# Kernel optimization log

Measured on AMD Instinct MI355X. Metric: run time of the kernel, lower is better.

## Reference

```python
import jax, jax.numpy as jnp
import numpy as np

B, S_SRC, T, D, H, DFF, NC, L = 8, 256, 64, 256, 8, 1024, 128, 2
HD = D // H
EPS = 1e-5


def _pe(length, d):
    pos = jnp.arange(length, dtype=jnp.float32)[:, None]
    div = jnp.exp(jnp.arange(0, d, 2, dtype=jnp.float32) * (-np.log(10000.0) / d))
    pe = jnp.zeros((length, d), dtype=jnp.float32)
    pe = pe.at[:, 0::2].set(jnp.sin(pos * div))
    pe = pe.at[:, 1::2].set(jnp.cos(pos * div))
    return pe


def setup_inputs() -> dict:
    key = jax.random.key(0)
    ks = jax.random.split(key, 16)
    s = 0.02
    rn = lambda k, shape: jax.random.normal(k, shape, dtype=jnp.float32) * s
    return {
        "encoder_output": jax.random.normal(ks[0], (B, S_SRC, D), dtype=jnp.float32),
        "emb_w": rn(ks[1], (D, NC)), "emb_b": jnp.zeros((D,), jnp.float32),
        "sa_wqkv": rn(ks[2], (L, 3 * D, D)), "sa_bqkv": jnp.zeros((L, 3 * D), jnp.float32),
        "sa_wo": rn(ks[3], (L, D, D)), "sa_bo": jnp.zeros((L, D), jnp.float32),
        "ca_wqkv": rn(ks[4], (L, 3 * D, D)), "ca_bqkv": jnp.zeros((L, 3 * D), jnp.float32),
        "ca_wo": rn(ks[5], (L, D, D)), "ca_bo": jnp.zeros((L, D), jnp.float32),
        "ln1_g": jnp.ones((L, D), jnp.float32), "ln1_b": jnp.zeros((L, D), jnp.float32),
        "ln2_g": jnp.ones((L, D), jnp.float32), "ln2_b": jnp.zeros((L, D), jnp.float32),
        "ffn_w1": rn(ks[6], (L, DFF, D)), "ffn_b1": jnp.zeros((L, DFF), jnp.float32),
        "ffn_w2": rn(ks[7], (L, D, DFF)), "ffn_b2": jnp.zeros((L, D), jnp.float32),
        "ln3_g": jnp.ones((L, D), jnp.float32), "ln3_b": jnp.zeros((L, D), jnp.float32),
        "op_w1": rn(ks[8], (D, D)), "op_b1": jnp.zeros((D,), jnp.float32),
        "bn_g": jnp.ones((D,), jnp.float32), "bn_b": jnp.zeros((D,), jnp.float32),
        "op_w2": rn(ks[9], (NC, D)), "op_b2": jnp.zeros((NC,), jnp.float32),
        "tgt_length": T,
    }


def _ln(x, g, b):
    m = x.mean(-1, keepdims=True)
    v = ((x - m) ** 2).mean(-1, keepdims=True)
    return (x - m) * jax.lax.rsqrt(v + EPS) * g + b


def _heads(x):  # [B,T,D] -> [B,H,T,HD]
    b, t, _ = x.shape
    return x.reshape(b, t, H, HD).transpose(0, 2, 1, 3)


def _merge(x):  # [B,H,T,HD] -> [B,T,D]
    return x.transpose(0, 2, 1, 3).reshape(x.shape[0], -1, D)


def _forward(encoder_output, emb_w, emb_b, sa_wqkv, sa_bqkv, sa_wo, sa_bo,
             ca_wqkv, ca_bqkv, ca_wo, ca_bo, ln1_g, ln1_b, ln2_g, ln2_b,
             ffn_w1, ffn_b1, ffn_w2, ffn_b2, ln3_g, ln3_b,
             op_w1, op_b1, bn_g, bn_b, op_w2, op_b2, tgt_length):
    Tq = tgt_length
    pe = _pe(Tq, D)
    scale = 1.0 / np.sqrt(HD)
    causal = jnp.where(jnp.arange(Tq)[:, None] >= jnp.arange(Tq)[None, :], 0.0, -1e9).astype(jnp.float32)
    # cross-attention K/V from encoder memory (constant across decode steps)
    mem_kv = jnp.einsum('bsd,led->lbse', encoder_output, ca_wqkv[:, D:, :]) + ca_bqkv[:, None, None, D:]
    mem_k = mem_kv[..., :D].reshape(L, B, S_SRC, H, HD).transpose(0, 1, 3, 2, 4)
    mem_v = mem_kv[..., D:].reshape(L, B, S_SRC, H, HD).transpose(0, 1, 3, 2, 4)

    def decode_full(buf):  # buf [B,Tq,NC] -> logits [B,Tq,NC]
        x = buf @ emb_w.T + emb_b + pe[None]
        for l in range(L):
            qkv = x @ sa_wqkv[l].T + sa_bqkv[l]
            q, k, v = (_heads(qkv[..., i * D:(i + 1) * D]) for i in range(3))
            att = jax.nn.softmax(jnp.einsum('bhqe,bhke->bhqk', q, k) * scale + causal, axis=-1)
            o = _merge(jnp.einsum('bhqk,bhke->bhqe', att, v)) @ sa_wo[l].T + sa_bo[l]
            x = _ln(x + o, ln1_g[l], ln1_b[l])
            qc = _heads(x @ ca_wqkv[l, :D].T + ca_bqkv[l, :D])
            attc = jax.nn.softmax(jnp.einsum('bhqe,bhke->bhqk', qc, mem_k[l]) * scale, axis=-1)
            oc = _merge(jnp.einsum('bhqk,bhke->bhqe', attc, mem_v[l])) @ ca_wo[l].T + ca_bo[l]
            x = _ln(x + oc, ln2_g[l], ln2_b[l])
            f = jax.nn.relu(x @ ffn_w1[l].T + ffn_b1[l]) @ ffn_w2[l].T + ffn_b2[l]
            x = _ln(x + f, ln3_g[l], ln3_b[l])
        y = x @ op_w1.T + op_b1
        # eval-mode BatchNorm1d with running stats (0, 1): pure affine
        y = jax.nn.relu(y * (1.0 / np.sqrt(1.0 + EPS)) * bn_g + bn_b)
        return y @ op_w2.T + op_b2

    def step(buf, t):
        out = decode_full(buf)                                   # [B,Tq,NC]
        y_t = jax.lax.dynamic_slice_in_dim(out, t, 1, axis=1)    # [B,1,NC]
        buf = jax.lax.dynamic_update_slice_in_dim(buf, y_t, jnp.minimum(t + 1, Tq - 1), axis=1)
        return buf, y_t[:, 0]

    buf0 = jnp.zeros((B, Tq, NC), dtype=jnp.float32)  # decoder_input starts as zeros
    _, ys = jax.lax.scan(step, buf0, jnp.arange(Tq))
    return ys.transpose(1, 0, 2)  # [B,Tq,NC]


def reference(encoder_output, emb_w, emb_b, sa_wqkv, sa_bqkv, sa_wo, sa_bo,
              ca_wqkv, ca_bqkv, ca_wo, ca_bo, ln1_g, ln1_b, ln2_g, ln2_b,
              ffn_w1, ffn_b1, ffn_w2, ffn_b2, ln3_g, ln3_b,
              op_w1, op_b1, bn_g, bn_b, op_w2, op_b2, tgt_length):
    return _forward(encoder_output, emb_w, emb_b, sa_wqkv, sa_bqkv, sa_wo, sa_bo,
                    ca_wqkv, ca_bqkv, ca_wo, ca_bo, ln1_g, ln1_b, ln2_g, ln2_b,
                    ffn_w1, ffn_b1, ffn_w2, ffn_b2, ln3_g, ln3_b,
                    op_w1, op_b1, bn_g, bn_b, op_w2, op_b2, tgt_length)
```

## Files before the change

### kernel.cpp

```cpp
#include <hip/hip_runtime.h>
#include <math.h>


#define EPS_ 1e-5f
#define SCALE_ 0.17677669529663687f
#define BNS 0.99999500003749969f
#define DEV __device__ __forceinline__
#define DYNF 36864

#define D4(a,b) ((a).x*(b).x+(a).y*(b).y+(a).z*(b).z+(a).w*(b).w)
#define F4(p)  (*(float4*)(p))
#define CF4(p) (*(const float4*)(p))

DEV float ald(const float* p){return __hip_atomic_load(p,__ATOMIC_RELAXED,__HIP_MEMORY_SCOPE_AGENT);}
DEV void  ast(float* p,float v){__hip_atomic_store(p,v,__ATOMIC_RELAXED,__HIP_MEMORY_SCOPE_AGENT);}
DEV int   aldi(const int* p){return __hip_atomic_load(p,__ATOMIC_RELAXED,__HIP_MEMORY_SCOPE_AGENT);}
DEV void  asti(int* p,int v){__hip_atomic_store(p,v,__ATOMIC_RELAXED,__HIP_MEMORY_SCOPE_AGENT);}

DEV float wsum(float v){
#pragma unroll
  for(int o=32;o;o>>=1) v+=__shfl_xor(v,o,64);
  return v;
}
DEV float wmax(float v){
#pragma unroll
  for(int o=32;o;o>>=1) v=fmaxf(v,__shfl_xor(v,o,64));
  return v;
}

DEV void waitflags(const int* base,int n,int s){
  if((int)threadIdx.x<64){
    const int* p=base+threadIdx.x*32;
    bool need=(int)threadIdx.x<n;
    int v=need?aldi(p):0x7fffffff;
    while(!__all(v>=s)){ v=need?aldi(p):0x7fffffff; }
  }
  __syncthreads();
}

template<int NB>
DEV void ln_reg(float (&v)[NB],const float* __restrict__ g,
                const float* __restrict__ bb,float* red){
  int tid=threadIdx.x,wid=tid>>6,lane=tid&63;
  float s[NB],s2[NB];
#pragma unroll
  for(int r=0;r<NB;++r){ s[r]=wsum(v[r]); s2[r]=wsum(v[r]*v[r]); }
  if(lane==0){
#pragma unroll
    for(int r=0;r<NB;++r){ red[r*4+wid]=s[r]; red[NB*4+r*4+wid]=s2[r]; }
  }
  __syncthreads();
  float gv=g[tid],bv=bb[tid];
#pragma unroll
  for(int r=0;r<NB;++r){
    float S=red[r*4+0]+red[r*4+1]+red[r*4+2]+red[r*4+3];
    float S2=red[NB*4+r*4+0]+red[NB*4+r*4+1]+red[NB*4+r*4+2]+red[NB*4+r*4+3];
    float m=S*(1.f/256.f);
    float rs=rsqrtf(S2*(1.f/256.f)-m*m+EPS_);
    v[r]=(v[r]-m)*rs*gv+bv;
  }
}

template<int NB,int L>
DEV void role_s1(float* LDS,int h,int bs,
    const float* __restrict__ sa_wqkv,const float* __restrict__ sa_bqkv,
    const float* __restrict__ sa_wo,
    const float* __restrict__ ln2_g,const float* __restrict__ ln2_b,
    const float* __restrict__ ln3_g,const float* __restrict__ ln3_b,
    const float* __restrict__ ffn_b2,const float* __restrict__ emb_b,
    int* F1,const int* F3,const int* FX0,
    float* kc,float* vc,const float* r2red,float* r3red,
    const float* p3,float* p1,const float* xrow){
  const int tid=threadIdx.x;
  float* W   =LDS;
  float* WO  =LDS+24960;
  float* XS  =LDS+34176;
  float* QKV =LDS+35200;
  float* SC  =LDS+35584;
  float* PART=LDS+35840;
  float* RED =LDS+36096;

  for(int idx=tid;idx<96*64;idx+=256){
    int row=idx>>6,i4=idx&63,which=row>>5,j=row&31;
    F4(&W[row*260+4*i4])=CF4(sa_wqkv+(size_t)L*196608+((size_t)(which*256+h*32+j))*256+4*i4);
  }
  for(int idx=tid;idx<256*8;idx+=256){
    int c=idx>>3,i=idx&7;
    F4(&WO[c*36+4*i])=CF4(sa_wo+(size_t)L*65536+(size_t)c*256+h*32+4*i);
  }
  __syncthreads();

  float dv=expf((float)(tid&~1)*(-9.210340371976184f/256.f));

  for(int t=0;t<64;++t){
    if(L==0){
      waitflags(FX0+bs*32,NB,t);
      float aarg=(float)t*dv;
      float peb=emb_b[tid]+((tid&1)?cosf(aarg):sinf(aarg));
#pragma unroll
      for(int bi=0;bi<NB;++bi) XS[bi*256+tid]=ald(xrow+(bs+bi)*256+tid)+peb;
      __syncthreads();
    }else{
      waitflags(F3+bs*16*32,NB*16,t+1);
      float r2v[NB],p3v[NB][16];
#pragma unroll
      for(int bi=0;bi<NB;++bi) r2v[bi]=ald(r2red+(bs+bi)*256+tid);
#pragma unroll
      for(int bi=0;bi<NB;++bi)
#pragma unroll
        for(int cg=0;cg<16;++cg) p3v[bi][cg]=ald(p3+(cg*8+bs+bi)*256+tid);
      ln_reg<NB>(r2v,ln2_g,ln2_b,RED);
      float r3v[NB];
      float fb=ffn_b2[tid];
#pragma unroll
      for(int bi=0;bi<NB;++bi){
        float s=0.f;
#pragma unroll
        for(int cg=0;cg<16;++cg) s+=p3v[bi][cg];
        r3v[bi]=r2v[bi]+s+fb;
        if(h==0) ast(r3red+(bs+bi)*256+tid,r3v[bi]);
      }
      ln_reg<NB>(r3v,ln3_g,ln3_b,RED+32);
#pragma unroll
      for(int bi=0;bi<NB;++bi) XS[bi*256+tid]=r3v[bi];
      __syncthreads();
    }
    if(tid<192){
      int row=tid>>1,kq=tid&1;
      float a[NB];
#pragma unroll
      for(int bi=0;bi<NB;++bi) a[bi]=0.f;
#pragma unroll
      for(int i=0;i<32;++i){
        float4 w=F4(&W[row*260+kq*128+4*i]);
#pragma unroll
        for(int bi=0;bi<NB;++bi) a[bi]+=D4(w,F4(&XS[bi*256+kq*128+4*i]));
      }
#pragma unroll
      for(int bi=0;bi<NB;++bi) a[bi]+=__shfl_down(a[bi],1,64);
      if(kq==0){
        int which=row>>5,j=row&31;
        float bias=sa_bqkv[L*768+which*256+h*32+j];
#pragma unroll
        for(int bi=0;bi<NB;++bi){
          float v=a[bi]+bias;
          if(which==0) QKV[bi*96+j]=v;
          else{
            int off=(which==1)?32:64;
            QKV[bi*96+off+j]=v;
            float* cache=(which==1)?kc:vc;
            cache[(((size_t)L*64+(bs+bi)*8+h)*64+t)*32+j]=v;
          }
        }
      }
    }
    __syncthreads();
    {
      int bi=(tid>>6)&(NB-1),key=tid&63;
      float s=-3.0e38f;
      if(key<=t){
        float a=0.f;
        if(key==t){
#pragma unroll
          for(int i=0;i<8;++i) a+=D4(F4(&QKV[bi*96+4*i]),F4(&QKV[bi*96+32+4*i]));
        }else{
          const float4* kr=(const float4*)(kc+(((size_t)L*64+(bs+bi)*8+h)*64+key)*32);
#pragma unroll
          for(int i=0;i<8;++i) a+=D4(F4(&QKV[bi*96+4*i]),kr[i]);
        }
        s=a*SCALE_;
      }
      float mx=wmax(s);
      float e=(key<=t)?expf(s-mx):0.f;
      float sm=wsum(e);
      SC[bi*64+key]=e/sm;
    }
    __syncthreads();
    {
      int bi=(tid>>6)&(NB-1),lane=tid&63,gg=lane>>5,col=lane&31;
      float acc=0.f;
      int k0=gg*32,k1=min(k0+32,t+1);
      for(int k=k0;k<k1;++k){
        float vv=(k==t)?QKV[bi*96+64+col]
                       :vc[(((size_t)L*64+(bs+bi)*8+h)*64+k)*32+col];
        acc+=SC[bi*64+k]*vv;
      }
      PART[bi*64+gg*32+col]=acc;
    }
    __syncthreads();
    if(tid<NB*32){
      int bi=tid>>5,col=tid&31;
      QKV[bi*96+col]=PART[bi*64+col]+PART[bi*64+32+col];
    }
    __syncthreads();
    {
      float a[NB];
#pragma unroll
      for(int bi=0;bi<NB;++bi) a[bi]=0.f;
#pragma unroll
      for(int i=0;i<8;++i){
        float4 w=F4(&WO[tid*36+4*i]);
#pragma unroll
        for(int bi=0;bi<NB;++bi) a[bi]+=D4(w,F4(&QKV[bi*96+4*i]));
      }
#pragma unroll
      for(int bi=0;bi<NB;++bi) ast(p1+(h*8+bs+bi)*256+tid,a[bi]);
    }
    __syncthreads();
    if(tid<NB) asti(F1+((L*8+bs+tid)*8+h)*32,t+1);
  }
}

DEV void role_s2(float* LDS,int rid,
    const float* __restrict__ enc,
    const float* __restrict__ ca_wqkv,const float* __restrict__ ca_bqkv,
    const float* __restrict__ ca_wo,
    const float* __restrict__ ln1_g,const float* __restrict__ ln1_b,
    const float* __restrict__ ln3_g,const float* __restrict__ ln3_b,
    const float* __restrict__ sa_bo,const float* __restrict__ emb_b,
    const int* F1,int* F2,
    const float* r3red,float* r1red,const float* p1,float* p2,const float* xrow){
  const int tid=threadIdx.x;
  const int b=rid>>4,h=(rid>>1)&7,l=rid&1;
  float* WQ  =LDS;
  float* WO  =LDS+8320;
  float* MK  =LDS+17536;
  float* MV  =LDS+26752;
  float* XS  =LDS+35968;
  float* PS  =LDS+36224;
  float* PART=LDS+36480;
  float* QC  =LDS+36736;
  float* RED =LDS+36784;

  for(int idx=tid;idx<64*64;idx+=256){
    int row=idx>>6,i4=idx&63;
    int grow=(row<32)?(256+h*32+row):(512+h*32+row-32);
    F4(&LDS[row*260+4*i4])=CF4(ca_wqkv+(size_t)l*196608+(size_t)grow*256+4*i4);
  }
  __syncthreads();
  for(int p=0;p<2;++p){
    int s=p*128+(tid>>1),kh=tid&1;
    float4 er[32];
#pragma unroll
    for(int i=0;i<32;++i) er[i]=CF4(enc+((size_t)(b*256+s))*256+kh*128+4*i);
    for(int out=0;out<64;++out){
      float a=0.f;
#pragma unroll
      for(int i=0;i<32;++i) a+=D4(F4(&LDS[out*260+kh*128+4*i]),er[i]);
      a+=__shfl_down(a,1,64);
      if(kh==0){
        if(out<32) MK[s*36+out]    =a+ca_bqkv[l*768+256+h*32+out];
        else       MV[s*36+out-32] =a+ca_bqkv[l*768+512+h*32+out-32];
      }
    }
  }
  __syncthreads();
  for(int idx=tid;idx<32*64;idx+=256){
    int row=idx>>6,i4=idx&63;
    F4(&WQ[row*260+4*i4])=CF4(ca_wqkv+(size_t)l*196608+(size_t)(h*32+row)*256+4*i4);
  }
  for(int idx=tid;idx<256*8;idx+=256){
    int c=idx>>3,i=idx&7;
    F4(&WO[c*36+4*i])=CF4(ca_wo+(size_t)l*65536+(size_t)c*256+h*32+4*i);
  }
  __syncthreads();

  float dv=expf((float)(tid&~1)*(-9.210340371976184f/256.f));

  for(int t=0;t<64;++t){
    waitflags(F1+(l*8+b)*8*32,8,t+1);
    float p1v[8];
#pragma unroll
    for(int h2=0;h2<8;++h2) p1v[h2]=ald(p1+(h2*8+b)*256+tid);
    float xv;
    if(l==0){
      float aarg=(float)t*dv;
      xv=ald(xrow+b*256+tid)+emb_b[tid]+((tid&1)?cosf(aarg):sinf(aarg));
    }else{
      float t0[1]={ald(r3red+b*256+tid)};
      ln_reg<1>(t0,ln3_g,ln3_b,RED);
      xv=t0[0];
    }
    float r1v=xv+sa_bo[l*256+tid];
#pragma unroll
    for(int h2=0;h2<8;++h2) r1v+=p1v[h2];
    if(h==0) ast(r1red+l*2048+b*256+tid,r1v);
    float t1[1]={r1v};
    ln_reg<1>(t1,ln1_g+l*256,ln1_b+l*256,RED+32);
    XS[tid]=t1[0];
    __syncthreads();
    {
      int col=tid>>3,g=tid&7;
      float a=0.f;
#pragma unroll
      for(int i=0;i<8;++i) a+=D4(F4(&WQ[col*260+g*32+4*i]),F4(&XS[g*32+4*i]));
      a+=__shfl_down(a,4,64);a+=__shfl_down(a,2,64);a+=__shfl_down(a,1,64);
      if(g==0) QC[col]=a+ca_bqkv[l*768+h*32+col];
    }
    __syncthreads();
    {
      float a=0.f;
#pragma unroll
      for(int i=0;i<8;++i) a+=D4(F4(&MK[tid*36+4*i]),F4(&QC[4*i]));
      float sv=a*SCALE_;
      int wid=tid>>6,lane=tid&63;
      float mx=wmax(sv);
      if(lane==0) RED[wid]=mx;
      __syncthreads();
      mx=fmaxf(fmaxf(RED[0],RED[1]),fmaxf(RED[2],RED[3]));
      float e=expf(sv-mx);
      float sm=wsum(e);
      if(lane==0) RED[4+wid]=sm;
      __syncthreads();
      sm=RED[4]+RED[5]+RED[6]+RED[7];
      PS[tid]=e/sm;
    }
    __syncthreads();
    {
      int gg=tid>>5,col=tid&31;
      float acc=0.f;
      for(int s2=gg*32;s2<gg*32+32;++s2) acc+=PS[s2]*MV[s2*36+col];
      PART[gg*32+col]=acc;
    }
    __syncthreads();
    if(tid<32){
      float o=0.f;
#pragma unroll
      for(int g2=0;g2<8;++g2) o+=PART[g2*32+tid];
      QC[tid]=o;
    }
    __syncthreads();
    {
      float a=0.f;
#pragma unroll
      for(int i=0;i<8;++i) a+=D4(F4(&WO[tid*36+4*i]),F4(&QC[4*i]));
      ast(p2+(h*8+b)*256+tid,a);
    }
    __syncthreads();
    if(tid==0) asti(F2+((l*8+b)*8+h)*32,t+1);
  }
}

DEV void role_s3(float* LDS,int rid,
    const float* __restrict__ ffn_w1,const float* __restrict__ ffn_b1,
    const float* __restrict__ ffn_w2,
    const float* __restrict__ ln1_g,const float* __restrict__ ln1_b,
    const float* __restrict__ ln2_g,const float* __restrict__ ln2_b,
    const float* __restrict__ ca_bo,
    const int* F2,int* F3,
    const float* r1red,float* r2red,const float* p2,float* p3){
  const int tid=threadIdx.x;
  const int l=rid>>5,cg=(rid>>1)&15,bh=rid&1,bs=bh*4;
  float* W1 =LDS;
  float* W2T=LDS+16640;
  float* X4 =LDS+33280;
  float* HH =LDS+34304;
  float* RED=LDS+34576;

  for(int idx=tid;idx<64*64;idx+=256){
    int row=idx>>6,i4=idx&63;
    F4(&W1[row*260+4*i4])=CF4(ffn_w1+(size_t)l*262144+(size_t)(cg*64+row)*256+4*i4);
  }
  for(int idx=tid;idx<256*16;idx+=256){
    int cc=idx>>4,k4=idx&15;
    float4 w=CF4(ffn_w2+(size_t)l*262144+(size_t)cc*1024+cg*64+4*k4);
    W2T[(4*k4+0)*260+cc]=w.x;W2T[(4*k4+1)*260+cc]=w.y;
    W2T[(4*k4+2)*260+cc]=w.z;W2T[(4*k4+3)*260+cc]=w.w;
  }
  __syncthreads();

  for(int t=0;t<64;++t){
    waitflags(F2+(l*8+bs)*8*32,32,t+1);
    float r1v[4],p2v[4][8];
#pragma unroll
    for(int bi=0;bi<4;++bi) r1v[bi]=ald(r1red+l*2048+(bs+bi)*256+tid);
#pragma unroll
    for(int bi=0;bi<4;++bi)
#pragma unroll
      for(int h2=0;h2<8;++h2) p2v[bi][h2]=ald(p2+(h2*8+bs+bi)*256+tid);
    ln_reg<4>(r1v,ln1_g+l*256,ln1_b+l*256,RED);
    float r2v[4];
    float cb=ca_bo[l*256+tid];
#pragma unroll
    for(int bi=0;bi<4;++bi){
      float s=0.f;
#pragma unroll
      for(int h2=0;h2<8;++h2) s+=p2v[bi][h2];
      r2v[bi]=r1v[bi]+s+cb;
      if(cg==0) ast(r2red+l*2048+(bs+bi)*256+tid,r2v[bi]);
    }
    ln_reg<4>(r2v,ln2_g+l*256,ln2_b+l*256,RED+32);
#pragma unroll
    for(int bi=0;bi<4;++bi) X4[bi*256+tid]=r2v[bi];
    __syncthreads();
    {
      int row=tid>>2,kq=tid&3;
      float a0=0.f,a1=0.f,a2=0.f,a3=0.f;
#pragma unroll
      for(int i=0;i<16;++i){
        float4 w=F4(&W1[row*260+kq*64+4*i]);
        a0+=D4(w,F4(&X4[0*256+kq*64+4*i]));a1+=D4(w,F4(&X4[1*256+kq*64+4*i]));
        a2+=D4(w,F4(&X4[2*256+kq*64+4*i]));a3+=D4(w,F4(&X4[3*256+kq*64+4*i]));
      }
      a0+=__shfl_down(a0,2,64);a0+=__shfl_down(a0,1,64);
      a1+=__shfl_down(a1,2,64);a1+=__shfl_down(a1,1,64);
      a2+=__shfl_down(a2,2,64);a2+=__shfl_down(a2,1,64);
      a3+=__shfl_down(a3,2,64);a3+=__shfl_down(a3,1,64);
      if(kq==0){
        float b1v=ffn_b1[l*1024+cg*64+row];
        HH[0*68+row]=fmaxf(a0+b1v,0.f);HH[1*68+row]=fmaxf(a1+b1v,0.f);
        HH[2*68+row]=fmaxf(a2+b1v,0.f);HH[3*68+row]=fmaxf(a3+b1v,0.f);
      }
    }
    __syncthreads();
    {
      int chunk=tid&63,bi=tid>>6;
      float ax=0.f,ay=0.f,az=0.f,aw=0.f;
      for(int k=0;k<64;++k){
        float4 w=F4(&W2T[k*260+4*chunk]);
        float hv=HH[bi*68+k];
        ax+=w.x*hv;ay+=w.y*hv;az+=w.z*hv;aw+=w.w*hv;
      }
      float* dst=p3+(size_t)l*32768+(size_t)(cg*8+bs+bi)*256+4*chunk;
      ast(dst+0,ax);ast(dst+1,ay);ast(dst+2,az);ast(dst+3,aw);
    }
    __syncthreads();
    if(tid<4) asti(F3+((l*8+bs+tid)*16+cg)*32,t+1);
  }
}

DEV void role_head(float* LDS,int b,
    const float* __restrict__ op_w1,const float* __restrict__ op_b1,
    const float* __restrict__ bn_g,const float* __restrict__ bn_b,
    const float* __restrict__ op_w2,const float* __restrict__ op_b2,
    const float* __restrict__ emb_w,
    const float* __restrict__ ln2_g,const float* __restrict__ ln2_b,
    const float* __restrict__ ln3_g,const float* __restrict__ ln3_b,
    const float* __restrict__ ffn_b2,
    const int* F3,int* FX0,
    const float* r2red,const float* p3,float* xrow,float* outp){
  const int tid=threadIdx.x;
  float* X  =LDS;
  float* Y  =LDS+256;
  float* LG =LDS+512;
  float* RED=LDS+768;

  for(int t=0;t<64;++t){
    waitflags(F3+(8+b)*16*32,16,t+1);
    float t0[1]={ald(r2red+2048+b*256+tid)};
    float p3v[16];
#pragma unroll
    for(int cg=0;cg<16;++cg) p3v[cg]=ald(p3+32768+(cg*8+b)*256+tid);
    ln_reg<1>(t0,ln2_g+256,ln2_b+256,RED);
    float r3=t0[0]+ffn_b2[256+tid];
#pragma unroll
    for(int cg=0;cg<16;++cg) r3+=p3v[cg];
    float t1[1]={r3};
    ln_reg<1>(t1,ln3_g+256,ln3_b+256,RED+32);
    X[tid]=t1[0];
    __syncthreads();
    {
      int g=tid&15,cc=tid>>4;
      for(int it=0;it<16;++it){
        int c2=it*16+cc;
        const float4* w4=(const float4*)(op_w1+(size_t)c2*256+g*16);
        const float4* x4=(const float4*)(X+g*16);
        float a=0.f;
#pragma unroll
        for(int i=0;i<4;++i) a+=D4(w4[i],x4[i]);
        a+=__shfl_down(a,8,64);a+=__shfl_down(a,4,64);
        a+=__shfl_down(a,2,64);a+=__shfl_down(a,1,64);
        if(g==0){
          float y=a+op_b1[c2];
          Y[c2]=fmaxf(y*BNS*bn_g[c2]+bn_b[c2],0.f);
        }
      }
    }
    __syncthreads();
    {
      int g=tid&15,cc=tid>>4;
      for(int it=0;it<8;++it){
        int c2=it*16+cc;
        const float4* w4=(const float4*)(op_w2+(size_t)c2*256+g*16);
        const float4* y4=(const float4*)(Y+g*16);
        float a=0.f;
#pragma unroll
        for(int i=0;i<4;++i) a+=D4(w4[i],y4[i]);
        a+=__shfl_down(a,8,64);a+=__shfl_down(a,4,64);
        a+=__shfl_down(a,2,64);a+=__shfl_down(a,1,64);
        if(g==0){
          float v=a+op_b2[c2];
          LG[c2]=v;
          outp[((size_t)b*64+t)*128+c2]=v;
        }
      }
    }
    __syncthreads();
    if(t<63){
      int g=tid&7,cc=tid>>3;
      for(int it=0;it<8;++it){
        int c2=it*32+cc;
        const float4* w4=(const float4*)(emb_w+(size_t)c2*128+g*16);
        const float4* l4=(const float4*)(LG+g*16);
        float a=0.f;
#pragma unroll
        for(int i=0;i<4;++i) a+=D4(w4[i],l4[i]);
        a+=__shfl_down(a,4,64);a+=__shfl_down(a,2,64);a+=__shfl_down(a,1,64);
        if(g==0) ast(xrow+b*256+c2,a);
      }
    }
    __syncthreads();
    if(tid==0) asti(FX0+b*32,t+1);
  }
}


__global__ void __launch_bounds__(256,1) k_decode(
    const float* enc,const float* emb_w,const float* emb_b,
    const float* sa_wqkv,const float* sa_bqkv,const float* sa_wo,const float* sa_bo,
    const float* ca_wqkv,const float* ca_bqkv,const float* ca_wo,const float* ca_bo,
    const float* ln1_g,const float* ln1_b,const float* ln2_g,const float* ln2_b,
    const float* ffn_w1,const float* ffn_b1,const float* ffn_w2,const float* ffn_b2,
    const float* ln3_g,const float* ln3_b,
    const float* op_w1,const float* op_b1,const float* bn_g,const float* bn_b,
    const float* op_w2,const float* op_b2,
    int* FX0,int* F1,int* F2,int* F3,
    float* xrow,float* kc,float* vc,float* r1red,float* r2red,float* r3red,
    float* p1,float* p2,float* p3,float* outp){
  __shared__ __align__(16) float LDS[DYNF];
  const int blk=blockIdx.x;
  if(blk<16){
    role_s1<4,0>(LDS,blk>>1,(blk&1)*4,sa_wqkv,sa_bqkv,sa_wo,ln2_g,ln2_b,ln3_g,ln3_b,
                 ffn_b2,emb_b,F1,F3,FX0,kc,vc,r2red,r3red,p3,p1,xrow);
  }else if(blk<48){
    int r=blk-16;
    role_s1<2,1>(LDS,r>>2,(r&3)*2,sa_wqkv,sa_bqkv,sa_wo,ln2_g,ln2_b,ln3_g,ln3_b,
                 ffn_b2,emb_b,F1,F3,FX0,kc,vc,r2red,r3red,p3,p1,xrow);
  }else if(blk<176){
    role_s2(LDS,blk-48,enc,ca_wqkv,ca_bqkv,ca_wo,ln1_g,ln1_b,ln3_g,ln3_b,sa_bo,emb_b,
            F1,F2,r3red,r1red,p1,p2,xrow);
  }else if(blk<240){
    role_s3(LDS,blk-176,ffn_w1,ffn_b1,ffn_w2,ln1_g,ln1_b,ln2_g,ln2_b,ca_bo,
            F2,F3,r1red,r2red,p2,p3);
  }else{
    role_head(LDS,blk-240,op_w1,op_b1,bn_g,bn_b,op_w2,op_b2,emb_w,
              ln2_g,ln2_b,ln3_g,ln3_b,ffn_b2,F3,FX0,r2red,p3,xrow,outp);
  }
}


extern "C" void kernel_launch(void* const* d_in, const int* in_sizes, int n_in,
                              void* d_out, int out_size, void* d_ws, size_t ws_size,
                              hipStream_t stream) {
  (void)in_sizes;(void)n_in;(void)out_size;(void)ws_size;
  const float* enc     =(const float*)d_in[0];
  const float* emb_w   =(const float*)d_in[1];
  const float* emb_b   =(const float*)d_in[2];
  const float* sa_wqkv =(const float*)d_in[3];
  const float* sa_bqkv =(const float*)d_in[4];
  const float* sa_wo   =(const float*)d_in[5];
  const float* sa_bo   =(const float*)d_in[6];
  const float* ca_wqkv =(const float*)d_in[7];
  const float* ca_bqkv =(const float*)d_in[8];
  const float* ca_wo   =(const float*)d_in[9];
  const float* ca_bo   =(const float*)d_in[10];
  const float* ln1_g   =(const float*)d_in[11];
  const float* ln1_b   =(const float*)d_in[12];
  const float* ln2_g   =(const float*)d_in[13];
  const float* ln2_b   =(const float*)d_in[14];
  const float* ffn_w1  =(const float*)d_in[15];
  const float* ffn_b1  =(const float*)d_in[16];
  const float* ffn_w2  =(const float*)d_in[17];
  const float* ffn_b2  =(const float*)d_in[18];
  const float* ln3_g   =(const float*)d_in[19];
  const float* ln3_b   =(const float*)d_in[20];
  const float* op_w1   =(const float*)d_in[21];
  const float* op_b1   =(const float*)d_in[22];
  const float* bn_g    =(const float*)d_in[23];
  const float* bn_b    =(const float*)d_in[24];
  const float* op_w2   =(const float*)d_in[25];
  const float* op_b2   =(const float*)d_in[26];

  float* out=(float*)d_out;

  int* I=(int*)d_ws;
  int* FX0=I;
  int* F1 =I+256;
  int* F2 =I+4352;
  int* F3 =I+8448;
  hipMemsetAsync(d_ws,0,16640*4+2048*4,stream);

  float* F=(float*)d_ws+16640;
  float* xrow =F;
  float* kc   =xrow+2048;
  float* vc   =kc+262144;
  float* r1red=vc+262144;
  float* r2red=r1red+4096;
  float* r3red=r2red+4096;
  float* p1   =r3red+2048;
  float* p2   =p1+16384;
  float* p3   =p2+16384;

  k_decode<<<248,256,0,stream>>>(
      enc,emb_w,emb_b,sa_wqkv,sa_bqkv,sa_wo,sa_bo,
      ca_wqkv,ca_bqkv,ca_wo,ca_bo,ln1_g,ln1_b,ln2_g,ln2_b,
      ffn_w1,ffn_b1,ffn_w2,ffn_b2,ln3_g,ln3_b,
      op_w1,op_b1,bn_g,bn_b,op_w2,op_b2,
      FX0,F1,F2,F3,
      xrow,kc,vc,r1red,r2red,r3red,p1,p2,p3,out);
}
```

Baseline: 3.806 ms.

## Add early residual-ready flags so stages overlap LayerNorm with partial-sum waits

Adds new flags (FER1/FER2/FER3) that the owning block raises as soon as the residual row (r1red/r2red/r3red) has been written. Downstream roles wait on these first and compute their LayerNorm of the residual before waiting on the slower full partial-sum flags. This hides LayerNorm and load latency behind the cross-block pipeline. The cross-attention softmax is also merged into a single pass, with per-wave max and sum combined afterwards, which removes one barrier. The cost is extra flag traffic, more syncthreads inside the h==0/cg==0 branches, and shifted RED offsets that must not collide.

```diff
diff --git a/kernel.cpp b/kernel.cpp
--- a/kernel.cpp
+++ b/kernel.cpp
@@ -68,7 +68,7 @@
     const float* __restrict__ ln2_g,const float* __restrict__ ln2_b,
     const float* __restrict__ ln3_g,const float* __restrict__ ln3_b,
     const float* __restrict__ ffn_b2,const float* __restrict__ emb_b,
-    int* F1,const int* F3,const int* FX0,
+    int* F1,const int* F3,const int* FX0,const int* FER2,int* FER3,
     float* kc,float* vc,const float* r2red,float* r3red,
     const float* p3,float* p1,const float* xrow){
   const int tid=threadIdx.x;
@@ -94,22 +94,24 @@
 
   for(int t=0;t<64;++t){
     if(L==0){
-      waitflags(FX0+bs*32,NB,t);
       float aarg=(float)t*dv;
       float peb=emb_b[tid]+((tid&1)?cosf(aarg):sinf(aarg));
+      waitflags(FX0+bs*32,NB,t);
 #pragma unroll
       for(int bi=0;bi<NB;++bi) XS[bi*256+tid]=ald(xrow+(bs+bi)*256+tid)+peb;
       __syncthreads();
     }else{
+      waitflags(FER2+bs*32,NB,t+1);
+      float r2v[NB];
+#pragma unroll
+      for(int bi=0;bi<NB;++bi) r2v[bi]=ald(r2red+(bs+bi)*256+tid);
+      ln_reg<NB>(r2v,ln2_g,ln2_b,RED);
       waitflags(F3+bs*16*32,NB*16,t+1);
-      float r2v[NB],p3v[NB][16];
-#pragma unroll
-      for(int bi=0;bi<NB;++bi) r2v[bi]=ald(r2red+(bs+bi)*256+tid);
+      float p3v[NB][16];
 #pragma unroll
       for(int bi=0;bi<NB;++bi)
 #pragma unroll
         for(int cg=0;cg<16;++cg) p3v[bi][cg]=ald(p3+(cg*8+bs+bi)*256+tid);
-      ln_reg<NB>(r2v,ln2_g,ln2_b,RED);
       float r3v[NB];
       float fb=ffn_b2[tid];
 #pragma unroll
@@ -118,7 +120,12 @@
 #pragma unroll
         for(int cg=0;cg<16;++cg) s+=p3v[bi][cg];
         r3v[bi]=r2v[bi]+s+fb;
-        if(h==0) ast(r3red+(bs+bi)*256+tid,r3v[bi]);
+      }
+      if(h==0){
+#pragma unroll
+        for(int bi=0;bi<NB;++bi) ast(r3red+(bs+bi)*256+tid,r3v[bi]);
+        __syncthreads();
+        if(tid<NB) asti(FER3+(bs+tid)*32,t+1);
       }
       ln_reg<NB>(r3v,ln3_g,ln3_b,RED+32);
 #pragma unroll
@@ -218,7 +225,7 @@
     const float* __restrict__ ln1_g,const float* __restrict__ ln1_b,
     const float* __restrict__ ln3_g,const float* __restrict__ ln3_b,
     const float* __restrict__ sa_bo,const float* __restrict__ emb_b,
-    const int* F1,int* F2,
+    const int* F1,int* F2,const int* FX0,const int* FER3,int* FER1,
     const float* r3red,float* r1red,const float* p1,float* p2,const float* xrow){
   const int tid=threadIdx.x;
   const int b=rid>>4,h=(rid>>1)&7,l=rid&1;
@@ -268,25 +275,32 @@
   float dv=expf((float)(tid&~1)*(-9.210340371976184f/256.f));
 
   for(int t=0;t<64;++t){
-    waitflags(F1+(l*8+b)*8*32,8,t+1);
-    float p1v[8];
-#pragma unroll
-    for(int h2=0;h2<8;++h2) p1v[h2]=ald(p1+(h2*8+b)*256+tid);
     float xv;
     if(l==0){
       float aarg=(float)t*dv;
-      xv=ald(xrow+b*256+tid)+emb_b[tid]+((tid&1)?cosf(aarg):sinf(aarg));
+      float peb=emb_b[tid]+((tid&1)?cosf(aarg):sinf(aarg));
+      waitflags(FX0+b*32,1,t);
+      xv=ald(xrow+b*256+tid)+peb;
     }else{
+      waitflags(FER3+b*32,1,t+1);
       float t0[1]={ald(r3red+b*256+tid)};
       ln_reg<1>(t0,ln3_g,ln3_b,RED);
       xv=t0[0];
     }
+    waitflags(F1+(l*8+b)*8*32,8,t+1);
+    float p1v[8];
+#pragma unroll
+    for(int h2=0;h2<8;++h2) p1v[h2]=ald(p1+(h2*8+b)*256+tid);
     float r1v=xv+sa_bo[l*256+tid];
 #pragma unroll
     for(int h2=0;h2<8;++h2) r1v+=p1v[h2];
-    if(h==0) ast(r1red+l*2048+b*256+tid,r1v);
+    if(h==0){
+      ast(r1red+l*2048+b*256+tid,r1v);
+      __syncthreads();
+      if(tid==0) asti(FER1+(l*8+b)*32,t+1);
+    }
     float t1[1]={r1v};
-    ln_reg<1>(t1,ln1_g+l*256,ln1_b+l*256,RED+32);
+    ln_reg<1>(t1,ln1_g+l*256,ln1_b+l*256,RED+8);
     XS[tid]=t1[0];
     __syncthreads();
     {
@@ -304,16 +318,15 @@
       for(int i=0;i<8;++i) a+=D4(F4(&MK[tid*36+4*i]),F4(&QC[4*i]));
       float sv=a*SCALE_;
       int wid=tid>>6,lane=tid&63;
-      float mx=wmax(sv);
-      if(lane==0) RED[wid]=mx;
+      float mw=wmax(sv);
+      float e=expf(sv-mw);
+      float sw=wsum(e);
+      if(lane==0){RED[16+wid]=mw;RED[20+wid]=sw;}
       __syncthreads();
-      mx=fmaxf(fmaxf(RED[0],RED[1]),fmaxf(RED[2],RED[3]));
-      float e=expf(sv-mx);
-      float sm=wsum(e);
-      if(lane==0) RED[4+wid]=sm;
-      __syncthreads();
-      sm=RED[4]+RED[5]+RED[6]+RED[7];
-      PS[tid]=e/sm;
+      float M=fmaxf(fmaxf(RED[16],RED[17]),fmaxf(RED[18],RED[19]));
+      float tot=RED[20]*expf(RED[16]-M)+RED[21]*expf(RED[17]-M)
+               +RED[22]*expf(RED[18]-M)+RED[23]*expf(RED[19]-M);
+      PS[tid]=e*expf(mw-M)/tot;
     }
     __syncthreads();
     {
@@ -347,7 +360,7 @@
     const float* __restrict__ ln1_g,const float* __restrict__ ln1_b,
     const float* __restrict__ ln2_g,const float* __restrict__ ln2_b,
     const float* __restrict__ ca_bo,
-    const int* F2,int* F3,
+    const int* F2,int* F3,const int* FER1,int* FER2,
     const float* r1red,float* r2red,const float* p2,float* p3){
   const int tid=threadIdx.x;
   const int l=rid>>5,cg=(rid>>1)&15,bh=rid&1,bs=bh*4;
@@ -370,15 +383,17 @@
   __syncthreads();
 
   for(int t=0;t<64;++t){
+    waitflags(FER1+(l*8+bs)*32,4,t+1);
+    float r1v[4];
+#pragma unroll
+    for(int bi=0;bi<4;++bi) r1v[bi]=ald(r1red+l*2048+(bs+bi)*256+tid);
+    ln_reg<4>(r1v,ln1_g+l*256,ln1_b+l*256,RED);
     waitflags(F2+(l*8+bs)*8*32,32,t+1);
-    float r1v[4],p2v[4][8];
-#pragma unroll
-    for(int bi=0;bi<4;++bi) r1v[bi]=ald(r1red+l*2048+(bs+bi)*256+tid);
+    float p2v[4][8];
 #pragma unroll
     for(int bi=0;bi<4;++bi)
 #pragma unroll
       for(int h2=0;h2<8;++h2) p2v[bi][h2]=ald(p2+(h2*8+bs+bi)*256+tid);
-    ln_reg<4>(r1v,ln1_g+l*256,ln1_b+l*256,RED);
     float r2v[4];
     float cb=ca_bo[l*256+tid];
 #pragma unroll
@@ -387,7 +402,12 @@
 #pragma unroll
       for(int h2=0;h2<8;++h2) s+=p2v[bi][h2];
       r2v[bi]=r1v[bi]+s+cb;
-      if(cg==0) ast(r2red+l*2048+(bs+bi)*256+tid,r2v[bi]);
+    }
+    if(cg==0){
+#pragma unroll
+      for(int bi=0;bi<4;++bi) ast(r2red+l*2048+(bs+bi)*256+tid,r2v[bi]);
+      __syncthreads();
+      if(tid<4) asti(FER2+(l*8+bs+tid)*32,t+1);
     }
     ln_reg<4>(r2v,ln2_g+l*256,ln2_b+l*256,RED+32);
 #pragma unroll
@@ -437,7 +457,7 @@
     const float* __restrict__ ln2_g,const float* __restrict__ ln2_b,
     const float* __restrict__ ln3_g,const float* __restrict__ ln3_b,
     const float* __restrict__ ffn_b2,
-    const int* F3,int* FX0,
+    const int* F3,int* FX0,const int* FER2,
     const float* r2red,const float* p3,float* xrow,float* outp){
   const int tid=threadIdx.x;
   float* X  =LDS;
@@ -446,17 +466,18 @@
   float* RED=LDS+768;
 
   for(int t=0;t<64;++t){
+    waitflags(FER2+(8+b)*32,1,t+1);
+    float t0[1]={ald(r2red+2048+b*256+tid)};
+    ln_reg<1>(t0,ln2_g+256,ln2_b+256,RED);
     waitflags(F3+(8+b)*16*32,16,t+1);
-    float t0[1]={ald(r2red+2048+b*256+tid)};
     float p3v[16];
 #pragma unroll
     for(int cg=0;cg<16;++cg) p3v[cg]=ald(p3+32768+(cg*8+b)*256+tid);
-    ln_reg<1>(t0,ln2_g+256,ln2_b+256,RED);
     float r3=t0[0]+ffn_b2[256+tid];
 #pragma unroll
     for(int cg=0;cg<16;++cg) r3+=p3v[cg];
     float t1[1]={r3};
-    ln_reg<1>(t1,ln3_g+256,ln3_b+256,RED+32);
+    ln_reg<1>(t1,ln3_g+256,ln3_b+256,RED+8);
     X[tid]=t1[0];
     __syncthreads();
     {
@@ -524,27 +545,27 @@
     const float* ln3_g,const float* ln3_b,
     const float* op_w1,const float* op_b1,const float* bn_g,const float* bn_b,
     const float* op_w2,const float* op_b2,
-    int* FX0,int* F1,int* F2,int* F3,
+    int* FX0,int* FER1,int* FER2,int* FER3,int* F1,int* F2,int* F3,
     float* xrow,float* kc,float* vc,float* r1red,float* r2red,float* r3red,
     float* p1,float* p2,float* p3,float* outp){
   __shared__ __align__(16) float LDS[DYNF];
   const int blk=blockIdx.x;
   if(blk<16){
     role_s1<4,0>(LDS,blk>>1,(blk&1)*4,sa_wqkv,sa_bqkv,sa_wo,ln2_g,ln2_b,ln3_g,ln3_b,
-                 ffn_b2,emb_b,F1,F3,FX0,kc,vc,r2red,r3red,p3,p1,xrow);
+                 ffn_b2,emb_b,F1,F3,FX0,FER2,FER3,kc,vc,r2red,r3red,p3,p1,xrow);
   }else if(blk<48){
     int r=blk-16;
     role_s1<2,1>(LDS,r>>2,(r&3)*2,sa_wqkv,sa_bqkv,sa_wo,ln2_g,ln2_b,ln3_g,ln3_b,
-                 ffn_b2,emb_b,F1,F3,FX0,kc,vc,r2red,r3red,p3,p1,xrow);
+                 ffn_b2,emb_b,F1,F3,FX0,FER2,FER3,kc,vc,r2red,r3red,p3,p1,xrow);
   }else if(blk<176){
     role_s2(LDS,blk-48,enc,ca_wqkv,ca_bqkv,ca_wo,ln1_g,ln1_b,ln3_g,ln3_b,sa_bo,emb_b,
-            F1,F2,r3red,r1red,p1,p2,xrow);
+            F1,F2,FX0,FER3,FER1,r3red,r1red,p1,p2,xrow);
   }else if(blk<240){
     role_s3(LDS,blk-176,ffn_w1,ffn_b1,ffn_w2,ln1_g,ln1_b,ln2_g,ln2_b,ca_bo,
-            F2,F3,r1red,r2red,p2,p3);
+            F2,F3,FER1,FER2,r1red,r2red,p2,p3);
   }else{
     role_head(LDS,blk-240,op_w1,op_b1,bn_g,bn_b,op_w2,op_b2,emb_w,
-              ln2_g,ln2_b,ln3_g,ln3_b,ffn_b2,F3,FX0,r2red,p3,xrow,outp);
+              ln2_g,ln2_b,ln3_g,ln3_b,ffn_b2,F3,FX0,FER2,r2red,p3,xrow,outp);
   }
 }
 
@@ -584,13 +605,16 @@
   float* out=(float*)d_out;
 
   int* I=(int*)d_ws;
-  int* FX0=I;
-  int* F1 =I+256;
-  int* F2 =I+4352;
-  int* F3 =I+8448;
-  hipMemsetAsync(d_ws,0,16640*4+2048*4,stream);
-
-  float* F=(float*)d_ws+16640;
+  int* FX0 =I;
+  int* FER1=I+256;
+  int* FER2=I+768;
+  int* FER3=I+1280;
+  int* F1  =I+1536;
+  int* F2  =I+5632;
+  int* F3  =I+9728;
+  hipMemsetAsync(d_ws,0,17920*4+2048*4,stream);
+
+  float* F=(float*)d_ws+17920;
   float* xrow =F;
   float* kc   =xrow+2048;
   float* vc   =kc+262144;
@@ -606,6 +630,6 @@
       ca_wqkv,ca_bqkv,ca_wo,ca_bo,ln1_g,ln1_b,ln2_g,ln2_b,
       ffn_w1,ffn_b1,ffn_w2,ffn_b2,ln3_g,ln3_b,
       op_w1,op_b1,bn_g,bn_b,op_w2,op_b2,
-      FX0,F1,F2,F3,
+      FX0,FER1,FER2,FER3,F1,F2,F3,
       xrow,kc,vc,r1red,r2red,r3red,p1,p2,p3,out);
 }
```

Result: faster. 3.607 ms (-5.2%).
